# Kernel tuning notes

Measured on AMD Instinct MI355X. Metric: run time of the kernel, lower is better.

Reference implementation:

```python
import jax, jax.numpy as jnp
import numpy as np

N, E, F, C, H, DK, CV, RH, B, OUT = 50000, 800000, 32, 64, 4, 32, 16, 16, 128, 64


def setup_inputs() -> dict:
    key = jax.random.key(0)
    ks = jax.random.split(key, 16)
    s = lambda k, shape, fan: jax.random.normal(k, shape, jnp.float32) / np.float32(np.sqrt(fan))
    return {
        'pos': jax.random.normal(ks[0], (N, 3), jnp.float32),
        'node_features': jax.random.normal(ks[1], (N, F), jnp.float32),
        'edge_index': jax.random.randint(ks[2], (2, E), 0, N),
        'batch': jnp.sort(jax.random.randint(ks[3], (N,), 0, B)),
        'W_emb': s(ks[4], (F, C), F), 'b_emb': jnp.zeros((C,), jnp.float32),
        'Wq': s(ks[5], (H, C, DK), C), 'Wk': s(ks[6], (H, C, DK), C),
        'Wv0': s(ks[7], (H, C, CV), C), 'Wv1': s(ks[8], (H, C, CV), C),
        'R1': s(ks[9], (H, 1, RH), 1), 'b1': jnp.zeros((H, RH), jnp.float32),
        'R2': s(ks[10], (H, RH, DK + 2 * CV), RH), 'b2': jnp.zeros((H, DK + 2 * CV), jnp.float32),
        'Wproj': s(ks[11], (H * CV, OUT), H * CV),
    }


def reference(pos, node_features, edge_index, batch, W_emb, b_emb, Wq, Wk, Wv0, Wv1, R1, b1, R2, b2, Wproj):
    src, dst = edge_index[0], edge_index[1]
    # relative positions, distances, normalized directions (= l=1 spherical harmonics)
    rel = pos[dst] - pos[src]                       # [E,3]
    d = jnp.linalg.norm(rel, axis=-1, keepdims=True) + 1e-8  # [E,1]
    Y1 = rel / d                                    # l=1 SH (unit direction); l=0 SH is constant
    # initial scalar embedding (torch.nn.Linear)
    h = node_features @ W_emb + b_emb               # [N,C]
    hs = h[src]                                     # [E,C] edge gather
    # per-head queries / radially-modulated keys
    q = jnp.einsum('nc,hck->hnk', h, Wq)            # [H,N,DK]
    ksrc = jnp.einsum('ec,hck->hek', hs, Wk)        # [H,E,DK]
    rh = jax.nn.silu(jnp.einsum('ei,hir->her', d, R1) + b1[:, None, :])  # radial MLP [H,E,RH]
    rout = jnp.einsum('her,hro->heo', rh, R2) + b2[:, None, :]           # [H,E,DK+2CV]
    rk, rv0, rv1 = rout[..., :DK], rout[..., DK:DK + CV], rout[..., DK + CV:]
    ke = ksrc * rk
    scores = jnp.einsum('hek,hek->he', q[:, dst], ke).T / np.float32(np.sqrt(DK))  # [E,H]
    # segment softmax over incoming edges of each destination node
    m = jax.ops.segment_max(scores, dst, num_segments=N)   # [N,H]
    ex = jnp.exp(scores - m[dst])
    denom = jax.ops.segment_sum(ex, dst, num_segments=N)
    alpha = ex / (denom[dst] + 1e-9)                       # [E,H]
    # equivariant values: scalar (0e) and vector (1o = scalar coeff * Y1) channels
    v0 = jnp.einsum('ec,hcv->ehv', hs, Wv0) * rv0.transpose(1, 0, 2)   # [E,H,CV]
    c1 = jnp.einsum('ec,hcv->ehv', hs, Wv1) * rv1.transpose(1, 0, 2)   # [E,H,CV]
    vec = c1[..., None] * Y1[:, None, None, :]                          # [E,H,CV,3]
    out0 = jax.ops.segment_sum(alpha[..., None] * v0, dst, num_segments=N)                       # [N,H,CV]
    out1 = jax.ops.segment_sum((alpha[..., None, None] * vec).reshape(E, H, CV * 3), dst, num_segments=N)  # [N,H,3CV]
    feat = jnp.concatenate([out0, out1], axis=-1)          # [N,H,4CV] per-head 16x0e+16x1o, concat over heads
    # global_add_pool by graph id
    pooled = jax.ops.segment_sum(feat, batch, num_segments=B)  # [B,H,4CV]
    # irrep-aware projection to 64x0e: only 0e channels contribute
    scal = pooled[:, :, :CV].reshape(B, H * CV)
    return scal @ Wproj
```

## Files before the change

kernel.cpp:

```cpp
#include <hip/hip_runtime.h>
#include <hip/hip_fp16.h>

static inline int idiv_up(long a, long b) { return (int)((a + b - 1) / b); }

#define RADIAL_G 2048
#define GBASE    (119 << 7)

typedef _Float16 h2 __attribute__((ext_vector_type(2)));

__device__ __forceinline__ unsigned pack_h2(float a, float b) {
    __half2 t = __floats2half2_rn(a, b);
    return *reinterpret_cast<unsigned*>(&t);
}
__device__ __forceinline__ unsigned pack_h1(float a) {
    __half t = __float2half_rn(a);
    return (unsigned)*reinterpret_cast<unsigned short*>(&t);
}
__device__ __forceinline__ h2 as_h2(unsigned u) {
    return *reinterpret_cast<h2*>(&u);
}
__device__ __forceinline__ _Float16 as_h1(unsigned u) {
    unsigned short s = (unsigned short)u;
    return *reinterpret_cast<_Float16*>(&s);
}
__device__ __forceinline__ float dot2(h2 a, h2 b) {
#if __has_builtin(__builtin_amdgcn_fdot2)
    return __builtin_amdgcn_fdot2(a, b, 0.f, false);
#else
    return (float)a.x * (float)b.x + (float)a.y * (float)b.y;
#endif
}

template <int CTRL>
__device__ __forceinline__ float dppf(float x) {
    return __int_as_float(__builtin_amdgcn_update_dpp(
        0, __float_as_int(x), CTRL, 0xF, 0xF, true));
}
__device__ __forceinline__ float row_allsum(float p) {
    p += dppf<0xB1>(p);
    p += dppf<0x4E>(p);
    p += dppf<0x124>(p);
    p += dppf<0x128>(p);
    return p;
}

#define FOLD_B 42
__global__ __launch_bounds__(256) void fold_and_count(
    const float* __restrict__ W_emb, const float* __restrict__ b_emb,
    const float* __restrict__ Wq, const float* __restrict__ Wk,
    const float* __restrict__ Wv0,
    float* __restrict__ Wcomb, float* __restrict__ bcomb,
    const int* __restrict__ ei, int* __restrict__ deg,
    unsigned short* __restrict__ rank, int Ee)
{
    if (blockIdx.x < FOLD_B) {
        int idx = blockIdx.x * 256 + threadIdx.x;
        if (idx >= 33 * 320) return;
        int row = idx / 320, j = idx - row * 320;
        float acc = 0.f;
        for (int c = 0; c < 64; ++c) {
            float w;
            if (j < 128)      { int h = j >> 5,         k = j & 31;         w = Wq [(h * 64 + c) * 32 + k]; }
            else if (j < 256) { int h = (j - 128) >> 5, k = (j - 128) & 31; w = Wk [(h * 64 + c) * 32 + k]; }
            else              { int h = (j - 256) >> 4, v = (j - 256) & 15; w = Wv0[(h * 64 + c) * 16 + v]; }
            float lhs = (row < 32) ? W_emb[row * 64 + c] : b_emb[c];
            acc += lhs * w;
        }
        if (row < 32) Wcomb[row * 320 + j] = acc;
        else          bcomb[j] = acc;
    } else {
        int e = (blockIdx.x - FOLD_B) * 256 + threadIdx.x;
        if (e >= Ee) return;
        int r = atomicAdd(&deg[ei[Ee + e]], 1);
        rank[e] = (unsigned short)r;
    }
}

__global__ __launch_bounds__(256) void node_qkv(
    const float* __restrict__ nf, const float* __restrict__ Wcomb,
    const float* __restrict__ bcomb, unsigned* __restrict__ Qt,
    unsigned* __restrict__ KVt, int Nn)
{
    int c    = blockIdx.x % 10;
    int tile = blockIdx.x / 10;
    int n = tile * 256 + threadIdx.x;
    bool valid = n < Nn;
    int nc = valid ? n : (Nn - 1);

    float nfv[32];
    const float4* nfp = (const float4*)(nf + (size_t)nc * 32);
#pragma unroll
    for (int f4 = 0; f4 < 8; ++f4) {
        float4 v = nfp[f4];
        nfv[f4 * 4 + 0] = v.x; nfv[f4 * 4 + 1] = v.y;
        nfv[f4 * 4 + 2] = v.z; nfv[f4 * 4 + 3] = v.w;
    }
    const float* Wc = Wcomb + c * 32;
    float acc[32];
#pragma unroll
    for (int j4 = 0; j4 < 8; ++j4) {
        float4 b = *(const float4*)&bcomb[c * 32 + j4 * 4];
        acc[j4 * 4 + 0] = b.x; acc[j4 * 4 + 1] = b.y;
        acc[j4 * 4 + 2] = b.z; acc[j4 * 4 + 3] = b.w;
    }
#pragma unroll
    for (int f = 0; f < 32; ++f) {
        float x = nfv[f];
        const float* row = Wc + f * 320;
#pragma unroll
        for (int j4 = 0; j4 < 8; ++j4) {
            float4 w = *(const float4*)&row[j4 * 4];
            acc[j4 * 4 + 0] = fmaf(x, w.x, acc[j4 * 4 + 0]);
            acc[j4 * 4 + 1] = fmaf(x, w.y, acc[j4 * 4 + 1]);
            acc[j4 * 4 + 2] = fmaf(x, w.z, acc[j4 * 4 + 2]);
            acc[j4 * 4 + 3] = fmaf(x, w.w, acc[j4 * 4 + 3]);
        }
    }
    if (!valid) return;
    if (c < 4) {
        unsigned* qp = Qt + (size_t)n * 64 + c * 16;
#pragma unroll
        for (int jj = 0; jj < 16; ++jj)
            qp[jj] = pack_h2(acc[jj], acc[jj + 16]);
    } else if (c < 8) {
        unsigned* kp = KVt + (size_t)n * 96 + (c - 4) * 16;
#pragma unroll
        for (int jj = 0; jj < 16; ++jj)
            kp[jj] = pack_h2(acc[jj], acc[jj + 16]);
    } else {
        unsigned short* vp = (unsigned short*)(KVt + (size_t)n * 96 + 64) + (c - 8) * 32;
#pragma unroll
        for (int jj = 0; jj < 32; ++jj)
            vp[jj] = (unsigned short)pack_h1(acc[jj]);
    }
}

__global__ __launch_bounds__(256) void calc_offs_hist(
    const int* __restrict__ deg, int* __restrict__ offs,
    int* __restrict__ gtot, int* __restrict__ ghist, int Nn)
{
    __shared__ int lh[128];
    if (threadIdx.x < 128) lh[threadIdx.x] = 0;
    __syncthreads();
    int n = blockIdx.x * 256 + threadIdx.x;
    int lane = threadIdx.x & 63;
    int d = (n < Nn) ? deg[n] : 0;
    int pre = d;
#pragma unroll
    for (int s = 1; s < 64; s <<= 1) {
        int t = __shfl_up(pre, s);
        if (lane >= s) pre += t;
    }
    int waveTot = __shfl(pre, 63);
    int base = 0;
    if (lane == 63) base = atomicAdd(gtot, waveTot);
    base = __shfl(base, 63);
    if (n < Nn) {
        offs[n] = base + pre - d;
        atomicAdd(&lh[min(d, 127)], 1);
    }
    __syncthreads();
    if (threadIdx.x < 128 && lh[threadIdx.x])
        atomicAdd(&ghist[threadIdx.x], lh[threadIdx.x]);
}

__global__ __launch_bounds__(128) void bin_scan(
    const int* __restrict__ ghist, int* __restrict__ bcur)
{
    __shared__ int s[128];
    s[threadIdx.x] = ghist[threadIdx.x];
    __syncthreads();
    int sum = 0;
    for (int b = threadIdx.x + 1; b < 128; ++b) sum += s[b];
    bcur[threadIdx.x] = sum;
}

__global__ __launch_bounds__(256) void scatter_perm_tab(
    const float* __restrict__ pos, const int* __restrict__ ei,
    const int* __restrict__ offs, const unsigned short* __restrict__ rank,
    int2* __restrict__ csr, int Ee,
    const int* __restrict__ deg, int* __restrict__ bcur,
    int* __restrict__ perm, int Nn,
    const float* __restrict__ R1, const float* __restrict__ b1,
    const float* __restrict__ R2, const float* __restrict__ b2,
    unsigned* __restrict__ TAB, int edgeB, int nodeB)
{
    int bx = blockIdx.x;
    if (bx < edgeB) {
        int e = bx * 256 + threadIdx.x;
        if (e >= Ee) return;
        int s  = ei[e];
        int dg = ei[Ee + e];
        float dx = pos[(size_t)dg * 3 + 0] - pos[(size_t)s * 3 + 0];
        float dy = pos[(size_t)dg * 3 + 1] - pos[(size_t)s * 3 + 1];
        float dz = pos[(size_t)dg * 3 + 2] - pos[(size_t)s * 3 + 2];
        float d = sqrtf(dx * dx + dy * dy + dz * dz) + 1e-8f;
        int p = offs[dg] + (int)rank[e];
        int2 pk; pk.x = s; pk.y = __float_as_int(d);
        csr[p] = pk;
        return;
    }
    bx -= edgeB;
    if (bx < nodeB) {
        __shared__ int lh[128], lbase[128];
        if (threadIdx.x < 128) lh[threadIdx.x] = 0;
        __syncthreads();
        int n = bx * 256 + threadIdx.x;
        int bk = -1, r = 0;
        if (n < Nn) {
            bk = min(deg[n], 127);
            r = atomicAdd(&lh[bk], 1);
        }
        __syncthreads();
        if (threadIdx.x < 128 && lh[threadIdx.x])
            lbase[threadIdx.x] = atomicAdd(&bcur[threadIdx.x], lh[threadIdx.x]);
        __syncthreads();
        if (n < Nn) perm[lbase[bk] + r] = n;
        return;
    }
    bx -= nodeB;
    {
        int idx = bx * 256 + threadIdx.x;
        if (idx >= RADIAL_G * 64) return;
        int g = idx >> 6, lane = idx & 63;
        int h = lane >> 4, j = lane & 15;
        float d = __uint_as_float(((unsigned)(g + GBASE) << 16) | 0x8000u);
        float rh[16];
#pragma unroll
        for (int r = 0; r < 16; ++r) {
            float x = fmaf(d, R1[h * 16 + r], b1[h * 16 + r]);
            rh[r] = x / (1.f + __expf(-x));
        }
        float rk0 = b2[h * 64 + j], rk1 = b2[h * 64 + j + 16], rv = b2[h * 64 + 32 + j];
#pragma unroll
        for (int r = 0; r < 16; ++r) {
            const float* row = R2 + (size_t)(h * 16 + r) * 64;
            rk0 = fmaf(rh[r], row[j], rk0);
            rk1 = fmaf(rh[r], row[j + 16], rk1);
            rv  = fmaf(rh[r], row[32 + j], rv);
        }
        const float rs = 0.17677669529663687f;
        TAB[(size_t)g * 128 + 2 * lane]     = pack_h2(rk0 * rs, rk1 * rs);
        TAB[(size_t)g * 128 + 2 * lane + 1] = pack_h1(rv);
    }
}

struct Pair {
    unsigned ku0, vu0, ku1, vu1;
    uint2 tb0, tb1;
};

__global__ __launch_bounds__(128) void node_attn(
    const unsigned* __restrict__ Qt, const unsigned* __restrict__ KVt,
    const uint2* __restrict__ TAB, const int2* __restrict__ csr,
    const int* __restrict__ offs, const int* __restrict__ deg,
    const int* __restrict__ batch, const int* __restrict__ perm,
    float* __restrict__ pooled, int Nn)
{
    int lane = threadIdx.x & 63;
    int wv = blockIdx.x * 2 + (threadIdx.x >> 6);
    if (wv >= Nn) return;
    int n = perm[wv];
    int start = offs[n], cnt = deg[n];
    if (cnt == 0) return;

    h2 qh = as_h2(Qt[(size_t)n * 64 + lane]);
    float l = 0.f, acc = 0.f;

    auto LD1 = [&](int ei, unsigned& ku, unsigned& vu, uint2& tb) {
        int2 pk = csr[ei];
        int g = (pk.y >> 16) - GBASE;
        g = min(max(g, 0), RADIAL_G - 1);
        tb = TAB[((size_t)g << 6) + lane];
        const unsigned* kb = KVt + (size_t)pk.x * 96;
        ku = kb[lane];
        vu = (unsigned)((const unsigned short*)(kb + 64))[lane];
    };
    auto LDP = [&](Pair& P, int ei) {
        LD1(ei,     P.ku0, P.vu0, P.tb0);
        LD1(ei + 1, P.ku1, P.vu1, P.tb1);
    };
    auto CMP1 = [&](unsigned ku, unsigned vu, uint2 tb) {
        h2 prod = as_h2(ku) * as_h2(tb.x);
        float p = dot2(qh, prod);
        p = row_allsum(p);
        float ex = __expf(fminf(p, 80.f));
        l += ex;
        float w = (float)(as_h1(vu) * as_h1(tb.y));
        acc = fmaf(ex, w, acc);
    };
    auto CMP = [&](const Pair& P) {
        CMP1(P.ku0, P.vu0, P.tb0);
        CMP1(P.ku1, P.vu1, P.tb1);
    };

    int e = start, end = start + cnt;
    Pair A, B, C;
    if (e + 5 < end) {
        LDP(A, e); LDP(B, e + 2); LDP(C, e + 4);
        for (; e + 7 < end; e += 2) {
            CMP(A);
            A = B; B = C;
            LDP(C, e + 6);
        }
        CMP(A); CMP(B); CMP(C);
        e += 6;
    }
    for (; e + 1 < end; e += 2) { LDP(A, e); CMP(A); }
    if (e < end) {
        unsigned ku, vu; uint2 tb;
        LD1(e, ku, vu, tb);
        CMP1(ku, vu, tb);
    }
    float o = acc / (l + 1e-30f);
    atomicAdd(&pooled[(size_t)batch[n] * 64 + lane], o);
}

__global__ __launch_bounds__(256) void final_proj(
    const float* __restrict__ pooled, const float* __restrict__ Wproj,
    float* __restrict__ out, int total)
{
    int idx = blockIdx.x * 256 + threadIdx.x;
    if (idx >= total) return;
    int b = idx >> 6, o = idx & 63;
    float acc = 0.f;
#pragma unroll
    for (int i = 0; i < 64; ++i) acc += pooled[b * 64 + i] * Wproj[i * 64 + o];
    out[idx] = acc;
}

extern "C" void kernel_launch(void* const* d_in, const int* in_sizes, int n_in,
                              void* d_out, int out_size, void* d_ws, size_t ws_size,
                              hipStream_t stream)
{
    const float* pos   = (const float*)d_in[0];
    const float* nf    = (const float*)d_in[1];
    const int*   ei    = (const int*)d_in[2];
    const int*   batch = (const int*)d_in[3];
    const float* W_emb = (const float*)d_in[4];
    const float* b_emb = (const float*)d_in[5];
    const float* Wq    = (const float*)d_in[6];
    const float* Wk    = (const float*)d_in[7];
    const float* Wv0   = (const float*)d_in[8];
    const float* R1    = (const float*)d_in[10];
    const float* b1    = (const float*)d_in[11];
    const float* R2    = (const float*)d_in[12];
    const float* b2    = (const float*)d_in[13];
    const float* Wproj = (const float*)d_in[14];
    float* out = (float*)d_out;

    long Nn = in_sizes[0] / 3;
    long Ee = in_sizes[2] / 2;
    int  Bb = out_size / 64;

    float* ws = (float*)d_ws;
    size_t o = 0;
    size_t WCOMB = o; o += 32 * 320;
    size_t BCOMB = o; o += 320;
    size_t QTAB  = o; o += (size_t)Nn * 64;
    size_t KVT   = o; o += (size_t)Nn * 96;
    size_t DEG   = o; o += (size_t)Nn;
    size_t GTOT  = o; o += 2;
    size_t GHIST = o; o += 128;
    size_t POOL  = o; o += (size_t)Bb * 64;
    size_t OFFS  = o; o += (size_t)Nn;
    size_t BCUR  = o; o += 128;
    size_t PERM  = o; o += (size_t)Nn;
    o = (o + 1) & ~(size_t)1;
    size_t CSR   = o; o += (size_t)Ee * 2;
    o = (o + 1) & ~(size_t)1;
    size_t TAB   = o; o += (size_t)RADIAL_G * 128;
    size_t RANK  = o; o += (Ee + 1) / 2;

    hipMemsetAsync(ws + DEG, 0,
                   ((size_t)Nn + 2 + 128 + (size_t)Bb * 64) * sizeof(float), stream);

    int edgeB = idiv_up(Ee, 256);
    int nodeB = idiv_up(Nn, 256);
    int tabB  = idiv_up(RADIAL_G * 64, 256);

    fold_and_count<<<FOLD_B + edgeB, 256, 0, stream>>>(
        W_emb, b_emb, Wq, Wk, Wv0, ws + WCOMB, ws + BCOMB,
        ei, (int*)(ws + DEG), (unsigned short*)(ws + RANK), (int)Ee);

    node_qkv<<<nodeB * 10, 256, 0, stream>>>(
        nf, ws + WCOMB, ws + BCOMB, (unsigned*)(ws + QTAB),
        (unsigned*)(ws + KVT), (int)Nn);

    calc_offs_hist<<<nodeB, 256, 0, stream>>>(
        (const int*)(ws + DEG), (int*)(ws + OFFS), (int*)(ws + GTOT),
        (int*)(ws + GHIST), (int)Nn);

    bin_scan<<<1, 128, 0, stream>>>(
        (const int*)(ws + GHIST), (int*)(ws + BCUR));

    scatter_perm_tab<<<edgeB + nodeB + tabB, 256, 0, stream>>>(
        pos, ei, (const int*)(ws + OFFS), (const unsigned short*)(ws + RANK),
        (int2*)(ws + CSR), (int)Ee,
        (const int*)(ws + DEG), (int*)(ws + BCUR), (int*)(ws + PERM), (int)Nn,
        R1, b1, R2, b2, (unsigned*)(ws + TAB), edgeB, nodeB);

    node_attn<<<idiv_up(Nn, 2), 128, 0, stream>>>(
        (const unsigned*)(ws + QTAB), (const unsigned*)(ws + KVT),
        (const uint2*)(ws + TAB), (const int2*)(ws + CSR),
        (const int*)(ws + OFFS), (const int*)(ws + DEG),
        batch, (const int*)(ws + PERM), ws + POOL, (int)Nn);

    final_proj<<<idiv_up(out_size, 256), 256, 0, stream>>>(
        ws + POOL, Wproj, out, out_size);
}
```

Baseline: 182.5 us.

## Pack CSR entries to 32 bits, pad KV rows, use exp2, unroll edge pipeline

Each CSR edge entry becomes one 32-bit word holding the source index (20 bits) and a precomputed radial-table bin (12 bits), so edge-list traffic halves and the bin computation moves out of the attention loop. KV rows are padded from 96 to 128 words so addresses come from a shift and rows align. The 1/ln2 factor is folded into the radial table so the kernel can call exp2f instead of __expf, and the three-deep load pipeline is unrolled to rotate buffers in place rather than copying them. The risks are that the 20-bit index only holds up to about 1M nodes, and the padded KV table takes more memory.

```diff
diff --git a/kernel.cpp b/kernel.cpp
--- a/kernel.cpp
+++ b/kernel.cpp
@@ -123,12 +123,12 @@
         for (int jj = 0; jj < 16; ++jj)
             qp[jj] = pack_h2(acc[jj], acc[jj + 16]);
     } else if (c < 8) {
-        unsigned* kp = KVt + (size_t)n * 96 + (c - 4) * 16;
+        unsigned* kp = KVt + ((size_t)n << 7) + (c - 4) * 16;
 #pragma unroll
         for (int jj = 0; jj < 16; ++jj)
             kp[jj] = pack_h2(acc[jj], acc[jj + 16]);
     } else {
-        unsigned short* vp = (unsigned short*)(KVt + (size_t)n * 96 + 64) + (c - 8) * 32;
+        unsigned short* vp = (unsigned short*)(KVt + ((size_t)n << 7) + 64) + (c - 8) * 32;
 #pragma unroll
         for (int jj = 0; jj < 32; ++jj)
             vp[jj] = (unsigned short)pack_h1(acc[jj]);
@@ -178,7 +178,7 @@
 __global__ __launch_bounds__(256) void scatter_perm_tab(
     const float* __restrict__ pos, const int* __restrict__ ei,
     const int* __restrict__ offs, const unsigned short* __restrict__ rank,
-    int2* __restrict__ csr, int Ee,
+    unsigned* __restrict__ csrp, int Ee,
     const int* __restrict__ deg, int* __restrict__ bcur,
     int* __restrict__ perm, int Nn,
     const float* __restrict__ R1, const float* __restrict__ b1,
@@ -195,9 +195,10 @@
         float dy = pos[(size_t)dg * 3 + 1] - pos[(size_t)s * 3 + 1];
         float dz = pos[(size_t)dg * 3 + 2] - pos[(size_t)s * 3 + 2];
         float d = sqrtf(dx * dx + dy * dy + dz * dz) + 1e-8f;
+        int g = (__float_as_int(d) >> 16) - GBASE;
+        g = min(max(g, 0), RADIAL_G - 1);
         int p = offs[dg] + (int)rank[e];
-        int2 pk; pk.x = s; pk.y = __float_as_int(d);
-        csr[p] = pk;
+        csrp[p] = (unsigned)s | ((unsigned)g << 20);
         return;
     }
     bx -= edgeB;
@@ -239,7 +240,7 @@
             rk1 = fmaf(rh[r], row[j + 16], rk1);
             rv  = fmaf(rh[r], row[32 + j], rv);
         }
-        const float rs = 0.17677669529663687f;
+        const float rs = 0.17677669529663687f * 1.4426950408889634f;
         TAB[(size_t)g * 128 + 2 * lane]     = pack_h2(rk0 * rs, rk1 * rs);
         TAB[(size_t)g * 128 + 2 * lane + 1] = pack_h1(rv);
     }
@@ -252,7 +253,7 @@
 
 __global__ __launch_bounds__(128) void node_attn(
     const unsigned* __restrict__ Qt, const unsigned* __restrict__ KVt,
-    const uint2* __restrict__ TAB, const int2* __restrict__ csr,
+    const uint2* __restrict__ TAB, const unsigned* __restrict__ csrp,
     const int* __restrict__ offs, const int* __restrict__ deg,
     const int* __restrict__ batch, const int* __restrict__ perm,
     float* __restrict__ pooled, int Nn)
@@ -268,11 +269,11 @@
     float l = 0.f, acc = 0.f;
 
     auto LD1 = [&](int ei, unsigned& ku, unsigned& vu, uint2& tb) {
-        int2 pk = csr[ei];
-        int g = (pk.y >> 16) - GBASE;
-        g = min(max(g, 0), RADIAL_G - 1);
+        unsigned pk = csrp[ei];
+        unsigned src = pk & 0xFFFFFu;
+        unsigned g   = pk >> 20;
         tb = TAB[((size_t)g << 6) + lane];
-        const unsigned* kb = KVt + (size_t)pk.x * 96;
+        const unsigned* kb = KVt + ((size_t)src << 7);
         ku = kb[lane];
         vu = (unsigned)((const unsigned short*)(kb + 64))[lane];
     };
@@ -284,7 +285,7 @@
         h2 prod = as_h2(ku) * as_h2(tb.x);
         float p = dot2(qh, prod);
         p = row_allsum(p);
-        float ex = __expf(fminf(p, 80.f));
+        float ex = exp2f(fminf(p, 110.f));
         l += ex;
         float w = (float)(as_h1(vu) * as_h1(tb.y));
         acc = fmaf(ex, w, acc);
@@ -298,10 +299,10 @@
     Pair A, B, C;
     if (e + 5 < end) {
         LDP(A, e); LDP(B, e + 2); LDP(C, e + 4);
-        for (; e + 7 < end; e += 2) {
-            CMP(A);
-            A = B; B = C;
-            LDP(C, e + 6);
+        for (; e + 11 < end; e += 6) {
+            CMP(A); LDP(A, e + 6);
+            CMP(B); LDP(B, e + 8);
+            CMP(C); LDP(C, e + 10);
         }
         CMP(A); CMP(B); CMP(C);
         e += 6;
@@ -358,7 +359,7 @@
     size_t WCOMB = o; o += 32 * 320;
     size_t BCOMB = o; o += 320;
     size_t QTAB  = o; o += (size_t)Nn * 64;
-    size_t KVT   = o; o += (size_t)Nn * 96;
+    size_t KVT   = o; o += (size_t)Nn * 128;
     size_t DEG   = o; o += (size_t)Nn;
     size_t GTOT  = o; o += 2;
     size_t GHIST = o; o += 128;
@@ -366,8 +367,7 @@
     size_t OFFS  = o; o += (size_t)Nn;
     size_t BCUR  = o; o += 128;
     size_t PERM  = o; o += (size_t)Nn;
-    o = (o + 1) & ~(size_t)1;
-    size_t CSR   = o; o += (size_t)Ee * 2;
+    size_t CSR   = o; o += (size_t)Ee;
     o = (o + 1) & ~(size_t)1;
     size_t TAB   = o; o += (size_t)RADIAL_G * 128;
     size_t RANK  = o; o += (Ee + 1) / 2;
@@ -396,13 +396,13 @@
 
     scatter_perm_tab<<<edgeB + nodeB + tabB, 256, 0, stream>>>(
         pos, ei, (const int*)(ws + OFFS), (const unsigned short*)(ws + RANK),
-        (int2*)(ws + CSR), (int)Ee,
+        (unsigned*)(ws + CSR), (int)Ee,
         (const int*)(ws + DEG), (int*)(ws + BCUR), (int*)(ws + PERM), (int)Nn,
         R1, b1, R2, b2, (unsigned*)(ws + TAB), edgeB, nodeB);
 
     node_attn<<<idiv_up(Nn, 2), 128, 0, stream>>>(
         (const unsigned*)(ws + QTAB), (const unsigned*)(ws + KVT),
-        (const uint2*)(ws + TAB), (const int2*)(ws + CSR),
+        (const uint2*)(ws + TAB), (const unsigned*)(ws + CSR),
         (const int*)(ws + OFFS), (const int*)(ws + DEG),
         batch, (const int*)(ws + PERM), ws + POOL, (int)Nn);
 
```

After: 182.3 us. Within noise of the previous version (-0.1%).
